# Optimization experiments

Hardware: AMD Instinct MI355X
Metric: run time of the kernel (lower is better)

Reference implementation:

```python
import jax, jax.numpy as jnp
import numpy as np


def setup_inputs() -> dict:
    key = jax.random.key(0)
    ks = jax.random.split(key, 8)
    B, C, H, W = 4, 256, 64, 64
    QP = 32  # query_planes = inplanes // 8
    x = jax.random.normal(ks[0], (B, C, H, W), dtype=jnp.float32)
    Wq = jax.random.normal(ks[1], (QP, C), dtype=jnp.float32) * (1.0 / np.sqrt(C))
    bq = jax.random.normal(ks[2], (QP,), dtype=jnp.float32) * 0.01
    Wk = jax.random.normal(ks[3], (QP, C), dtype=jnp.float32) * (1.0 / np.sqrt(C))
    bk = jax.random.normal(ks[4], (QP,), dtype=jnp.float32) * 0.01
    Wv = jax.random.normal(ks[5], (C, C), dtype=jnp.float32) * (1.0 / np.sqrt(C))
    bv = jax.random.normal(ks[6], (C,), dtype=jnp.float32) * 0.01
    gamma = jax.random.normal(ks[7], (), dtype=jnp.float32)
    return {"x": x, "Wq": Wq, "bq": bq, "Wk": Wk, "bk": bk,
            "Wv": Wv, "bv": bv, "gamma": gamma}


def reference(x, Wq, bq, Wk, bk, Wv, bv, gamma):
    B, C, H, W = x.shape
    N = H * W
    flat = x.reshape(B, C, N)                              # [B, C, N]
    # 1x1 Conv1d == pointwise linear over channel dim
    q = jnp.einsum('qc,bcn->bnq', Wq, flat) + bq[None, None, :]   # [B, N, QP] (already permuted)
    k = jnp.einsum('qc,bcn->bqn', Wk, flat) + bk[None, :, None]   # [B, QP, N]
    v = jnp.einsum('oc,bcn->bon', Wv, flat) + bv[None, :, None]   # [B, C, N]
    # scores[b, i, j] = <q_i, k_j>, NO 1/sqrt(d) scaling (as in source)
    scores = jnp.einsum('biq,bqj->bij', q, k)              # [B, N, N]
    # unusual softmax axis: dim=1 == over query positions i, per column j
    attn = jax.nn.softmax(scores, axis=1)                  # [B, N, N]
    out_attn = jnp.einsum('bcn,bnj->bcj', v, attn)         # [B, C, N]
    out_attn = out_attn.reshape(B, C, H, W)
    return gamma * out_attn + x
```

## Files before the change

### kernel.cpp

```cpp
#include <hip/hip_runtime.h>
#include <hip/hip_bf16.h>
#include <math.h>


#define NBATCH 4
#define CDIM   256
#define NSEQ   4096
#define QPDIM  32
#define LOG2E  1.44269504088896340736f

typedef _Float16 half8_t  __attribute__((ext_vector_type(8)));
typedef _Float16 half2_t  __attribute__((ext_vector_type(2)));
typedef float    floatx4  __attribute__((ext_vector_type(4)));
typedef float    floatx16 __attribute__((ext_vector_type(16)));

union H8 { half8_t h8; half2_t h2[4]; int i32[4]; };

__device__ inline half2_t pack_f16(float a, float b) {
    return __builtin_bit_cast(half2_t, __builtin_amdgcn_cvt_pkrtz(a, b));
}

__global__ __launch_bounds__(256) void wprep_kernel(
    const float* __restrict__ Wv, const float* __restrict__ Wq,
    const float* __restrict__ Wk, _Float16* __restrict__ wH)
{
    const int idx = blockIdx.x * 256 + threadIdx.x;
    const int e = idx * 8;
    const int r = e >> 8, c = e & 255;
    const float* src;
    float scale = 1.0f;
    if (r < 256)      src = Wv + (size_t)r * 256 + c;
    else if (r < 288) { src = Wq + (size_t)(r - 256) * 256 + c; scale = LOG2E; }
    else              src = Wk + (size_t)(r - 288) * 256 + c;
    float4 f0 = ((const float4*)src)[0];
    float4 f1 = ((const float4*)src)[1];
    half8_t h;
    h[0] = (_Float16)(f0.x * scale); h[1] = (_Float16)(f0.y * scale);
    h[2] = (_Float16)(f0.z * scale); h[3] = (_Float16)(f0.w * scale);
    h[4] = (_Float16)(f1.x * scale); h[5] = (_Float16)(f1.y * scale);
    h[6] = (_Float16)(f1.z * scale); h[7] = (_Float16)(f1.w * scale);
    *(half8_t*)(wH + (size_t)r * 256 + c) = h;
}

__global__ __launch_bounds__(256, 2) void qkv_kernel(
    const float* __restrict__ x, const _Float16* __restrict__ wH,
    const float* __restrict__ bq, const float* __restrict__ bk,
    const float* __restrict__ bv,
    _Float16* __restrict__ qH, _Float16* __restrict__ kH,
    _Float16* __restrict__ vHT)
{
    __shared__ _Float16 xT[32][264];

    const int blk  = blockIdx.x;
    const int slot = blk & 7;
    const int b    = slot >> 1;
    const int n0   = (((blk >> 3) << 1) | (slot & 1)) << 5;
    const int t    = threadIdx.x;
    const int w    = t >> 6;
    const int lane = t & 63;
    const int quad = lane >> 4;
    const int col  = lane & 15;

    {
        const int crow0 = t >> 3;
        const int npart = t & 7;
        #pragma unroll
        for (int pass = 0; pass < 8; ++pass) {
            const int c = pass * 32 + crow0;
            float4 f = *(const float4*)(
                x + ((size_t)(b * CDIM + c)) * NSEQ + n0 + npart * 4);
            xT[npart * 4 + 0][c] = (_Float16)f.x;
            xT[npart * 4 + 1][c] = (_Float16)f.y;
            xT[npart * 4 + 2][c] = (_Float16)f.z;
            xT[npart * 4 + 3][c] = (_Float16)f.w;
        }
    }
    __syncthreads();

    const int r0 = w * 80;
    floatx4 acc[5][2];
    #pragma unroll
    for (int mt = 0; mt < 5; ++mt)
        #pragma unroll
        for (int nt = 0; nt < 2; ++nt)
            acc[mt][nt] = (floatx4){0.f, 0.f, 0.f, 0.f};

    #pragma unroll
    for (int ks = 0; ks < 8; ++ks) {
        half8_t bf[2];
        #pragma unroll
        for (int nt = 0; nt < 2; ++nt)
            bf[nt] = *(const half8_t*)&xT[nt * 16 + col][ks * 32 + quad * 8];
        #pragma unroll
        for (int mt = 0; mt < 5; ++mt) {
            half8_t a = *(const half8_t*)(
                wH + (size_t)(r0 + mt * 16 + col) * 256 + ks * 32 + quad * 8);
            #pragma unroll
            for (int nt = 0; nt < 2; ++nt)
                acc[mt][nt] = __builtin_amdgcn_mfma_f32_16x16x32_f16(
                    a, bf[nt], acc[mt][nt], 0, 0, 0);
        }
    }

    #pragma unroll
    for (int mt = 0; mt < 5; ++mt) {
        const int gbase = r0 + mt * 16;
        const float* bp; int rl; float bscale = 1.0f;
        if (gbase < 256)      { bp = bv; rl = gbase; }
        else if (gbase < 288) { bp = bq; rl = gbase - 256; bscale = LOG2E; }
        else                  { bp = bk; rl = gbase - 288; }
        #pragma unroll
        for (int reg = 0; reg < 4; ++reg) {
            const int rr = rl + quad * 4 + reg;
            const float bias = bp[rr] * bscale;
            #pragma unroll
            for (int nt = 0; nt < 2; ++nt) {
                const int n = n0 + nt * 16 + col;
                const float val = acc[mt][nt][reg] + bias;
                if (gbase < 256)
                    vHT[((size_t)(b * CDIM + rr)) * NSEQ + n] = (_Float16)val;
                else if (gbase < 288)
                    qH[((size_t)(b * NSEQ + n)) * QPDIM + rr] = (_Float16)val;
                else
                    kH[((size_t)(b * NSEQ + n)) * QPDIM + rr] = (_Float16)val;
            }
        }
    }
}

__global__ __launch_bounds__(256, 4) void mpass_kernel(
    const _Float16* __restrict__ qH, const _Float16* __restrict__ kH,
    float* __restrict__ ms4)
{
    __shared__ float wmax[4][32];

    const int blk  = blockIdx.x;
    const int slot = blk & 7;
    const int b    = slot >> 1;
    const int idx  = ((blk >> 3) << 1) | (slot & 1);
    const int jblk = idx & 63;
    const int iq   = idx >> 6;
    const int t    = threadIdx.x;
    const int w    = t >> 6;
    const int lane = t & 63;
    const int l5   = lane >> 5;
    const int lj   = lane & 31;
    const int jt   = w & 1, ih = w >> 1;

    const _Float16* qg = qH + (size_t)b * NSEQ * QPDIM;
    const int j = jblk * 64 + jt * 32 + lj;
    const half8_t kb0 = *(const half8_t*)(
        kH + ((size_t)(b * NSEQ + j)) * QPDIM + l5 * 8);
    const half8_t kb1 = *(const half8_t*)(
        kH + ((size_t)(b * NSEQ + j)) * QPDIM + 16 + l5 * 8);

    float mx = -1e30f;
    const int ibase = iq * 1024 + ih * 512;
    for (int cc = 0; cc < 16; ++cc) {
        const _Float16* qp = qg + (size_t)(ibase + cc * 32 + lj) * QPDIM + l5 * 8;
        half8_t qa0 = *(const half8_t*)qp;
        half8_t qa1 = *(const half8_t*)(qp + 16);
        floatx16 S = __builtin_amdgcn_mfma_f32_32x32x16_f16(
            qa0, kb0, (floatx16){0.f}, 0, 0, 0);
        S = __builtin_amdgcn_mfma_f32_32x32x16_f16(qa1, kb1, S, 0, 0, 0);
        #pragma unroll
        for (int r = 0; r < 16; ++r) mx = fmaxf(mx, S[r]);
    }
    mx = fmaxf(mx, __shfl_xor(mx, 32));
    if (lane < 32) wmax[w][lane] = mx;
    __syncthreads();
    if (t < 64) {
        const int jt3 = t >> 5, c = t & 31;
        ms4[(size_t)iq * (NBATCH * NSEQ) + (size_t)b * NSEQ
            + jblk * 64 + jt3 * 32 + c] = fmaxf(wmax[jt3][c], wmax[jt3 + 2][c]);
    }
}

__global__ __launch_bounds__(512, 1) void attn_kernel(
    const _Float16* __restrict__ qH, const _Float16* __restrict__ kH,
    const _Float16* __restrict__ vHT, const float* __restrict__ ms4,
    const float* __restrict__ x, const float* __restrict__ gamma,
    float* __restrict__ out)
{
    __shared__ _Float16 vbuf[2][32768];
    __shared__ float lred[2][4][32];

    const int blk  = blockIdx.x;
    const int slot = blk & 7;
    const int b    = slot >> 1;
    const int jblk = ((blk >> 3) << 1) | (slot & 1);
    const int j0   = jblk << 6;
    const int t    = threadIdx.x;
    const int w    = t >> 6;
    const int lane = t & 63;
    const int l5   = lane >> 5;
    const int lj   = lane & 31;
    const int jh   = w & 1;
    const int ih   = w >> 1;

    const _Float16* qg = qH + (size_t)b * NSEQ * QPDIM;
    const _Float16* vg = vHT + (size_t)b * CDIM * NSEQ;

    const int jme = j0 + jh * 32 + lj;
    const half8_t kb0 = *(const half8_t*)(
        kH + ((size_t)(b * NSEQ + jme)) * QPDIM + l5 * 8);
    const half8_t kb1 = *(const half8_t*)(
        kH + ((size_t)(b * NSEQ + jme)) * QPDIM + 16 + l5 * 8);
    const float* msb = ms4 + (size_t)b * NSEQ + jme;
    const float mfix = fmaxf(
        fmaxf(msb[0], msb[NBATCH * NSEQ]),
        fmaxf(msb[2 * NBATCH * NSEQ], msb[3 * NBATCH * NSEQ]));
    floatx16 Sinit;
    #pragma unroll
    for (int r = 0; r < 16; ++r) Sinit[r] = -mfix;

    floatx16 acc[8];
    #pragma unroll
    for (int ct = 0; ct < 8; ++ct) acc[ct] = (floatx16){0.f};
    float lp = 0.0f;

    #define DMA_V(i0_, buf_)                                                   \
        {                                                                      \
            _Pragma("unroll")                                                  \
            for (int g = 0; g < 8; ++g) {                                      \
                const int uu = w * 512 + g * 64 + lane;                        \
                const int cl = uu >> 4;                                        \
                const int ck = (uu & 15) ^ (cl & 7);                           \
                const _Float16* src =                                          \
                    vg + (size_t)cl * NSEQ + (i0_) + ck * 8;                   \
                __builtin_amdgcn_global_load_lds(                              \
                    (const __attribute__((address_space(1))) void*)src,        \
                    (__attribute__((address_space(3))) void*)                  \
                        (&vbuf[buf_][(w * 512 + g * 64) * 8]),                 \
                    16, 0, 0);                                                 \
            }                                                                  \
        }

    DMA_V(0, 0);
    const _Float16* qb = qg + (size_t)(ih * 32 + lj) * QPDIM + l5 * 8;
    half8_t qa0 = *(const half8_t*)(qb);
    half8_t qa1 = *(const half8_t*)(qb + 16);

    int cur = 0;
    for (int i0 = 0; i0 < NSEQ; i0 += 128) {
        __syncthreads();
        if (i0 + 128 < NSEQ) DMA_V(i0 + 128, cur ^ 1);

        floatx16 S = __builtin_amdgcn_mfma_f32_32x32x16_f16(
            qa0, kb0, Sinit, 0, 0, 0);
        S = __builtin_amdgcn_mfma_f32_32x32x16_f16(qa1, kb1, S, 0, 0, 0);

        H8 lo, hi;
        float ls = 0.0f;
        #pragma unroll
        for (int p = 0; p < 4; ++p) {
            float pa = __builtin_amdgcn_exp2f(S[2 * p]);
            float pb = __builtin_amdgcn_exp2f(S[2 * p + 1]);
            ls += pa + pb;
            lo.h2[p] = pack_f16(pa, pb);
        }
        #pragma unroll
        for (int p = 0; p < 4; ++p) {
            float pa = __builtin_amdgcn_exp2f(S[8 + 2 * p]);
            float pb = __builtin_amdgcn_exp2f(S[8 + 2 * p + 1]);
            ls += pa + pb;
            hi.h2[p] = pack_f16(pa, pb);
        }
        lp += ls;

        H8 P0, P1;
#if __has_builtin(__builtin_amdgcn_permlane32_swap)
        {
            auto r0p = __builtin_amdgcn_permlane32_swap(
                (unsigned)lo.i32[0], (unsigned)lo.i32[2], false, false);
            P0.i32[0] = (int)r0p[0]; P0.i32[2] = (int)r0p[1];
            auto r1p = __builtin_amdgcn_permlane32_swap(
                (unsigned)lo.i32[1], (unsigned)lo.i32[3], false, false);
            P0.i32[1] = (int)r1p[0]; P0.i32[3] = (int)r1p[1];
            auto r2p = __builtin_amdgcn_permlane32_swap(
                (unsigned)hi.i32[0], (unsigned)hi.i32[2], false, false);
            P1.i32[0] = (int)r2p[0]; P1.i32[2] = (int)r2p[1];
            auto r3p = __builtin_amdgcn_permlane32_swap(
                (unsigned)hi.i32[1], (unsigned)hi.i32[3], false, false);
            P1.i32[1] = (int)r3p[0]; P1.i32[3] = (int)r3p[1];
        }
#else
        {
            H8 shl, shh;
            #pragma unroll
            for (int r = 0; r < 4; ++r) {
                shl.i32[r] = __shfl_xor(lo.i32[r], 32);
                shh.i32[r] = __shfl_xor(hi.i32[r], 32);
            }
            const bool high = (l5 != 0);
            P0.i32[0] = high ? shl.i32[2] : lo.i32[0];
            P0.i32[1] = high ? shl.i32[3] : lo.i32[1];
            P0.i32[2] = high ? lo.i32[2]  : shl.i32[0];
            P0.i32[3] = high ? lo.i32[3]  : shl.i32[1];
            P1.i32[0] = high ? shh.i32[2] : hi.i32[0];
            P1.i32[1] = high ? shh.i32[3] : hi.i32[1];
            P1.i32[2] = high ? hi.i32[2]  : shh.i32[0];
            P1.i32[3] = high ? hi.i32[3]  : shh.i32[1];
        }
#endif

        __builtin_amdgcn_s_setprio(1);
        #pragma unroll
        for (int ct = 0; ct < 8; ++ct) {
            const int cl = ct * 32 + lj;
            const int ic0 = (ih * 4 + 0 + l5) ^ (cl & 7);
            const int ic1 = (ih * 4 + 2 + l5) ^ (cl & 7);
            half8_t va0 = *(const half8_t*)&vbuf[cur][(cl * 16 + ic0) * 8];
            half8_t va1 = *(const half8_t*)&vbuf[cur][(cl * 16 + ic1) * 8];
            acc[ct] = __builtin_amdgcn_mfma_f32_32x32x16_f16(
                va0, P0.h8, acc[ct], 0, 0, 0);
            acc[ct] = __builtin_amdgcn_mfma_f32_32x32x16_f16(
                va1, P1.h8, acc[ct], 0, 0, 0);
        }
        __builtin_amdgcn_s_setprio(0);

        if (i0 + 128 < NSEQ) {
            qa0 = *(const half8_t*)(qb + (size_t)(i0 + 128) * QPDIM);
            qa1 = *(const half8_t*)(qb + (size_t)(i0 + 128) * QPDIM + 16);
        }
        cur ^= 1;
    }

    lp += __shfl_xor(lp, 32);
    if (lane < 32) lred[jh][ih][lane] = lp;
    __syncthreads();

    float* fred = (float*)vbuf;
    const int rA = jh * 2 + (ih >> 1);
    if (ih & 1) {
        float* rg = fred + rA * 8192;
        #pragma unroll
        for (int ct = 0; ct < 8; ++ct)
            #pragma unroll
            for (int reg = 0; reg < 16; ++reg) {
                const int crow = (reg & 3) + 8 * (reg >> 2) + 4 * l5;
                rg[(ct * 32 + crow) * 32 + lj] = acc[ct][reg];
            }
    }
    __syncthreads();
    if (!(ih & 1)) {
        float* rg = fred + rA * 8192;
        #pragma unroll
        for (int ct = 0; ct < 8; ++ct)
            #pragma unroll
            for (int reg = 0; reg < 16; ++reg) {
                const int crow = (reg & 3) + 8 * (reg >> 2) + 4 * l5;
                acc[ct][reg] += rg[(ct * 32 + crow) * 32 + lj];
            }
    }
    __syncthreads();
    if (ih == 0) {
        float* rg = fred + (jh * 2 + 0) * 8192;
        #pragma unroll
        for (int ct = 4; ct < 8; ++ct)
            #pragma unroll
            for (int reg = 0; reg < 16; ++reg) {
                const int crow = (reg & 3) + 8 * (reg >> 2) + 4 * l5;
                rg[(ct * 32 + crow) * 32 + lj] = acc[ct][reg];
            }
    } else if (ih == 2) {
        float* rg = fred + (jh * 2 + 1) * 8192;
        #pragma unroll
        for (int ct = 0; ct < 4; ++ct)
            #pragma unroll
            for (int reg = 0; reg < 16; ++reg) {
                const int crow = (reg & 3) + 8 * (reg >> 2) + 4 * l5;
                rg[(ct * 32 + crow) * 32 + lj] = acc[ct][reg];
            }
    }
    __syncthreads();
    if (ih == 0) {
        const float lsum = lred[jh][0][lj] + lred[jh][1][lj]
                         + lred[jh][2][lj] + lred[jh][3][lj];
        const float rv = gamma[0] / lsum;
        float* rg = fred + (jh * 2 + 1) * 8192;
        #pragma unroll
        for (int ct = 0; ct < 4; ++ct) {
            #pragma unroll
            for (int reg = 0; reg < 16; ++reg) {
                const int crow = (reg & 3) + 8 * (reg >> 2) + 4 * l5;
                const int c_ = ct * 32 + crow;
                const size_t off = ((size_t)(b * CDIM + c_)) * NSEQ + jme;
                const float sum =
                    acc[ct][reg] + rg[(ct * 32 + crow) * 32 + lj];
                out[off] = sum * rv + x[off];
            }
        }
    } else if (ih == 2) {
        const float lsum = lred[jh][0][lj] + lred[jh][1][lj]
                         + lred[jh][2][lj] + lred[jh][3][lj];
        const float rv = gamma[0] / lsum;
        float* rg = fred + (jh * 2 + 0) * 8192;
        #pragma unroll
        for (int ct = 4; ct < 8; ++ct) {
            #pragma unroll
            for (int reg = 0; reg < 16; ++reg) {
                const int crow = (reg & 3) + 8 * (reg >> 2) + 4 * l5;
                const int c_ = ct * 32 + crow;
                const size_t off = ((size_t)(b * CDIM + c_)) * NSEQ + jme;
                const float sum =
                    acc[ct][reg] + rg[(ct * 32 + crow) * 32 + lj];
                out[off] = sum * rv + x[off];
            }
        }
    }
}

extern "C" void kernel_launch(void* const* d_in, const int* in_sizes, int n_in,
                              void* d_out, int out_size, void* d_ws, size_t ws_size,
                              hipStream_t stream) {
    const float* x     = (const float*)d_in[0];
    const float* Wq    = (const float*)d_in[1];
    const float* bq    = (const float*)d_in[2];
    const float* Wk    = (const float*)d_in[3];
    const float* bk    = (const float*)d_in[4];
    const float* Wv    = (const float*)d_in[5];
    const float* bv    = (const float*)d_in[6];
    const float* gamma = (const float*)d_in[7];
    float* out = (float*)d_out;

    _Float16* w16 = (_Float16*)d_ws;
    _Float16* qH  = w16;
    _Float16* kH  = qH + (size_t)NBATCH * NSEQ * QPDIM;
    _Float16* vHT = kH + (size_t)NBATCH * NSEQ * QPDIM;
    _Float16* wH  = vHT + (size_t)NBATCH * CDIM * NSEQ;
    float*    ms4 = (float*)(wH + (size_t)320 * 256);

    wprep_kernel<<<40, 256, 0, stream>>>(Wv, Wq, Wk, wH);
    qkv_kernel<<<512, 256, 0, stream>>>(x, wH, bq, bk, bv, qH, kH, vHT);
    mpass_kernel<<<1024, 256, 0, stream>>>(qH, kH, ms4);
    attn_kernel<<<256, 512, 0, stream>>>(qH, kH, vHT, ms4, x, gamma, out);
}
```

Before: 163.7 us.

## Give each warp a private V slice and drop block barriers in attention loop

```diff
diff --git a/kernel.cpp b/kernel.cpp
--- a/kernel.cpp
+++ b/kernel.cpp
@@ -18,6 +18,44 @@
 
 __device__ inline half2_t pack_f16(float a, float b) {
     return __builtin_bit_cast(half2_t, __builtin_amdgcn_cvt_pkrtz(a, b));
+}
+
+__device__ inline void transformP(const H8& lo, const H8& hi,
+                                  H8& P0, H8& P1, const int l5) {
+#if __has_builtin(__builtin_amdgcn_permlane32_swap)
+    {
+        auto r0p = __builtin_amdgcn_permlane32_swap(
+            (unsigned)lo.i32[0], (unsigned)lo.i32[2], false, false);
+        P0.i32[0] = (int)r0p[0]; P0.i32[2] = (int)r0p[1];
+        auto r1p = __builtin_amdgcn_permlane32_swap(
+            (unsigned)lo.i32[1], (unsigned)lo.i32[3], false, false);
+        P0.i32[1] = (int)r1p[0]; P0.i32[3] = (int)r1p[1];
+        auto r2p = __builtin_amdgcn_permlane32_swap(
+            (unsigned)hi.i32[0], (unsigned)hi.i32[2], false, false);
+        P1.i32[0] = (int)r2p[0]; P1.i32[2] = (int)r2p[1];
+        auto r3p = __builtin_amdgcn_permlane32_swap(
+            (unsigned)hi.i32[1], (unsigned)hi.i32[3], false, false);
+        P1.i32[1] = (int)r3p[0]; P1.i32[3] = (int)r3p[1];
+    }
+#else
+    {
+        H8 shl, shh;
+        #pragma unroll
+        for (int r = 0; r < 4; ++r) {
+            shl.i32[r] = __shfl_xor(lo.i32[r], 32);
+            shh.i32[r] = __shfl_xor(hi.i32[r], 32);
+        }
+        const bool high = (l5 != 0);
+        P0.i32[0] = high ? shl.i32[2] : lo.i32[0];
+        P0.i32[1] = high ? shl.i32[3] : lo.i32[1];
+        P0.i32[2] = high ? lo.i32[2]  : shl.i32[0];
+        P0.i32[3] = high ? lo.i32[3]  : shl.i32[1];
+        P1.i32[0] = high ? shh.i32[2] : hi.i32[0];
+        P1.i32[1] = high ? shh.i32[3] : hi.i32[1];
+        P1.i32[2] = high ? hi.i32[2]  : shh.i32[0];
+        P1.i32[3] = high ? hi.i32[3]  : shh.i32[1];
+    }
+#endif
 }
 
 __global__ __launch_bounds__(256) void wprep_kernel(
@@ -183,7 +221,7 @@
     float* __restrict__ out)
 {
     __shared__ _Float16 vbuf[2][32768];
-    __shared__ float lred[2][4][32];
+    __shared__ float lred[4][64];
 
     const int blk  = blockIdx.x;
     const int slot = blk & 7;
@@ -195,39 +233,49 @@
     const int lane = t & 63;
     const int l5   = lane >> 5;
     const int lj   = lane & 31;
-    const int jh   = w & 1;
+    const int ch   = w & 1;
     const int ih   = w >> 1;
 
     const _Float16* qg = qH + (size_t)b * NSEQ * QPDIM;
     const _Float16* vg = vHT + (size_t)b * CDIM * NSEQ;
 
-    const int jme = j0 + jh * 32 + lj;
-    const half8_t kb0 = *(const half8_t*)(
-        kH + ((size_t)(b * NSEQ + jme)) * QPDIM + l5 * 8);
-    const half8_t kb1 = *(const half8_t*)(
-        kH + ((size_t)(b * NSEQ + jme)) * QPDIM + 16 + l5 * 8);
-    const float* msb = ms4 + (size_t)b * NSEQ + jme;
-    const float mfix = fmaxf(
-        fmaxf(msb[0], msb[NBATCH * NSEQ]),
-        fmaxf(msb[2 * NBATCH * NSEQ], msb[3 * NBATCH * NSEQ]));
-    floatx16 Sinit;
+    const int jme0 = j0 + lj;
+    const int jme1 = j0 + 32 + lj;
+    const half8_t kbA0 = *(const half8_t*)(
+        kH + ((size_t)(b * NSEQ + jme0)) * QPDIM + l5 * 8);
+    const half8_t kbB0 = *(const half8_t*)(
+        kH + ((size_t)(b * NSEQ + jme0)) * QPDIM + 16 + l5 * 8);
+    const half8_t kbA1 = *(const half8_t*)(
+        kH + ((size_t)(b * NSEQ + jme1)) * QPDIM + l5 * 8);
+    const half8_t kbB1 = *(const half8_t*)(
+        kH + ((size_t)(b * NSEQ + jme1)) * QPDIM + 16 + l5 * 8);
+
+    const float* msb0 = ms4 + (size_t)b * NSEQ + jme0;
+    const float mf0 = fmaxf(
+        fmaxf(msb0[0], msb0[NBATCH * NSEQ]),
+        fmaxf(msb0[2 * NBATCH * NSEQ], msb0[3 * NBATCH * NSEQ]));
+    const float* msb1 = ms4 + (size_t)b * NSEQ + jme1;
+    const float mf1 = fmaxf(
+        fmaxf(msb1[0], msb1[NBATCH * NSEQ]),
+        fmaxf(msb1[2 * NBATCH * NSEQ], msb1[3 * NBATCH * NSEQ]));
+
+    floatx16 acc[4][2];
     #pragma unroll
-    for (int r = 0; r < 16; ++r) Sinit[r] = -mfix;
-
-    floatx16 acc[8];
-    #pragma unroll
-    for (int ct = 0; ct < 8; ++ct) acc[ct] = (floatx16){0.f};
-    float lp = 0.0f;
+    for (int ct = 0; ct < 4; ++ct)
+        #pragma unroll
+        for (int jt = 0; jt < 2; ++jt) acc[ct][jt] = (floatx16){0.f};
+    float lp0 = 0.0f, lp1 = 0.0f;
 
     #define DMA_V(i0_, buf_)                                                   \
         {                                                                      \
             _Pragma("unroll")                                                  \
             for (int g = 0; g < 8; ++g) {                                      \
-                const int uu = w * 512 + g * 64 + lane;                        \
-                const int cl = uu >> 4;                                        \
-                const int ck = (uu & 15) ^ (cl & 7);                           \
+                const int uu = g * 64 + lane;                                  \
+                const int cl = uu >> 2;                                        \
+                const int ck = (uu & 3) ^ ((cl >> 1) & 3);                     \
                 const _Float16* src =                                          \
-                    vg + (size_t)cl * NSEQ + (i0_) + ck * 8;                   \
+                    vg + (size_t)(ch * 128 + cl) * NSEQ + (i0_) + ih * 32      \
+                       + ck * 8;                                               \
                 __builtin_amdgcn_global_load_lds(                              \
                     (const __attribute__((address_space(1))) void*)src,        \
                     (__attribute__((address_space(3))) void*)                  \
@@ -243,81 +291,93 @@
 
     int cur = 0;
     for (int i0 = 0; i0 < NSEQ; i0 += 128) {
-        __syncthreads();
-        if (i0 + 128 < NSEQ) DMA_V(i0 + 128, cur ^ 1);
-
-        floatx16 S = __builtin_amdgcn_mfma_f32_32x32x16_f16(
-            qa0, kb0, Sinit, 0, 0, 0);
-        S = __builtin_amdgcn_mfma_f32_32x32x16_f16(qa1, kb1, S, 0, 0, 0);
-
-        H8 lo, hi;
-        float ls = 0.0f;
-        #pragma unroll
-        for (int p = 0; p < 4; ++p) {
-            float pa = __builtin_amdgcn_exp2f(S[2 * p]);
-            float pb = __builtin_amdgcn_exp2f(S[2 * p + 1]);
-            ls += pa + pb;
-            lo.h2[p] = pack_f16(pa, pb);
-        }
-        #pragma unroll
-        for (int p = 0; p < 4; ++p) {
-            float pa = __builtin_amdgcn_exp2f(S[8 + 2 * p]);
-            float pb = __builtin_amdgcn_exp2f(S[8 + 2 * p + 1]);
-            ls += pa + pb;
-            hi.h2[p] = pack_f16(pa, pb);
-        }
-        lp += ls;
-
-        H8 P0, P1;
-#if __has_builtin(__builtin_amdgcn_permlane32_swap)
+        if (i0 + 128 < NSEQ) {
+            DMA_V(i0 + 128, cur ^ 1);
+            asm volatile("s_waitcnt vmcnt(8)" ::: "memory");
+        } else {
+            asm volatile("s_waitcnt vmcnt(0)" ::: "memory");
+        }
+        __builtin_amdgcn_sched_barrier(0);
+
+        half8_t va[4][2];
+        #pragma unroll
+        for (int ct = 0; ct < 4; ++ct) {
+            const int clr = ct * 32 + lj;
+            const int sw  = (clr >> 1) & 3;
+            va[ct][0] = *(const half8_t*)
+                &vbuf[cur][(w * 512 + clr * 4 + ((0 + l5) ^ sw)) * 8];
+            va[ct][1] = *(const half8_t*)
+                &vbuf[cur][(w * 512 + clr * 4 + ((2 + l5) ^ sw)) * 8];
+        }
+
+        floatx16 S0 = __builtin_amdgcn_mfma_f32_32x32x16_f16(
+            qa0, kbA0, (floatx16){0.f}, 0, 0, 0);
+        S0 = __builtin_amdgcn_mfma_f32_32x32x16_f16(qa1, kbB0, S0, 0, 0, 0);
+        floatx16 S1 = __builtin_amdgcn_mfma_f32_32x32x16_f16(
+            qa0, kbA1, (floatx16){0.f}, 0, 0, 0);
+        S1 = __builtin_amdgcn_mfma_f32_32x32x16_f16(qa1, kbB1, S1, 0, 0, 0);
+
         {
-            auto r0p = __builtin_amdgcn_permlane32_swap(
-                (unsigned)lo.i32[0], (unsigned)lo.i32[2], false, false);
-            P0.i32[0] = (int)r0p[0]; P0.i32[2] = (int)r0p[1];
-            auto r1p = __builtin_amdgcn_permlane32_swap(
-                (unsigned)lo.i32[1], (unsigned)lo.i32[3], false, false);
-            P0.i32[1] = (int)r1p[0]; P0.i32[3] = (int)r1p[1];
-            auto r2p = __builtin_amdgcn_permlane32_swap(
-                (unsigned)hi.i32[0], (unsigned)hi.i32[2], false, false);
-            P1.i32[0] = (int)r2p[0]; P1.i32[2] = (int)r2p[1];
-            auto r3p = __builtin_amdgcn_permlane32_swap(
-                (unsigned)hi.i32[1], (unsigned)hi.i32[3], false, false);
-            P1.i32[1] = (int)r3p[0]; P1.i32[3] = (int)r3p[1];
-        }
-#else
+            H8 lo, hi;
+            float ls = 0.0f;
+            #pragma unroll
+            for (int p = 0; p < 4; ++p) {
+                float pa = __builtin_amdgcn_exp2f(S0[2 * p]     - mf0);
+                float pb = __builtin_amdgcn_exp2f(S0[2 * p + 1] - mf0);
+                ls += pa + pb;
+                lo.h2[p] = pack_f16(pa, pb);
+            }
+            #pragma unroll
+            for (int p = 0; p < 4; ++p) {
+                float pa = __builtin_amdgcn_exp2f(S0[8 + 2 * p]     - mf0);
+                float pb = __builtin_amdgcn_exp2f(S0[8 + 2 * p + 1] - mf0);
+                ls += pa + pb;
+                hi.h2[p] = pack_f16(pa, pb);
+            }
+            lp0 += ls;
+            H8 Pa, Pb;
+            transformP(lo, hi, Pa, Pb, l5);
+            __builtin_amdgcn_s_setprio(1);
+            #pragma unroll
+            for (int ct = 0; ct < 4; ++ct) {
+                acc[ct][0] = __builtin_amdgcn_mfma_f32_32x32x16_f16(
+                    va[ct][0], Pa.h8, acc[ct][0], 0, 0, 0);
+                acc[ct][0] = __builtin_amdgcn_mfma_f32_32x32x16_f16(
+                    va[ct][1], Pb.h8, acc[ct][0], 0, 0, 0);
+            }
+            __builtin_amdgcn_s_setprio(0);
+        }
+
         {
-            H8 shl, shh;
-            #pragma unroll
-            for (int r = 0; r < 4; ++r) {
-                shl.i32[r] = __shfl_xor(lo.i32[r], 32);
-                shh.i32[r] = __shfl_xor(hi.i32[r], 32);
-            }
-            const bool high = (l5 != 0);
-            P0.i32[0] = high ? shl.i32[2] : lo.i32[0];
-            P0.i32[1] = high ? shl.i32[3] : lo.i32[1];
-            P0.i32[2] = high ? lo.i32[2]  : shl.i32[0];
-            P0.i32[3] = high ? lo.i32[3]  : shl.i32[1];
-            P1.i32[0] = high ? shh.i32[2] : hi.i32[0];
-            P1.i32[1] = high ? shh.i32[3] : hi.i32[1];
-            P1.i32[2] = high ? hi.i32[2]  : shh.i32[0];
-            P1.i32[3] = high ? hi.i32[3]  : shh.i32[1];
-        }
-#endif
-
-        __builtin_amdgcn_s_setprio(1);
-        #pragma unroll
-        for (int ct = 0; ct < 8; ++ct) {
-            const int cl = ct * 32 + lj;
-            const int ic0 = (ih * 4 + 0 + l5) ^ (cl & 7);
-            const int ic1 = (ih * 4 + 2 + l5) ^ (cl & 7);
-            half8_t va0 = *(const half8_t*)&vbuf[cur][(cl * 16 + ic0) * 8];
-            half8_t va1 = *(const half8_t*)&vbuf[cur][(cl * 16 + ic1) * 8];
-            acc[ct] = __builtin_amdgcn_mfma_f32_32x32x16_f16(
-                va0, P0.h8, acc[ct], 0, 0, 0);
-            acc[ct] = __builtin_amdgcn_mfma_f32_32x32x16_f16(
-                va1, P1.h8, acc[ct], 0, 0, 0);
-        }
-        __builtin_amdgcn_s_setprio(0);
+            H8 lo, hi;
+            float ls = 0.0f;
+            #pragma unroll
+            for (int p = 0; p < 4; ++p) {
+                float pa = __builtin_amdgcn_exp2f(S1[2 * p]     - mf1);
+                float pb = __builtin_amdgcn_exp2f(S1[2 * p + 1] - mf1);
+                ls += pa + pb;
+                lo.h2[p] = pack_f16(pa, pb);
+            }
+            #pragma unroll
+            for (int p = 0; p < 4; ++p) {
+                float pa = __builtin_amdgcn_exp2f(S1[8 + 2 * p]     - mf1);
+                float pb = __builtin_amdgcn_exp2f(S1[8 + 2 * p + 1] - mf1);
+                ls += pa + pb;
+                hi.h2[p] = pack_f16(pa, pb);
+            }
+            lp1 += ls;
+            H8 Pa, Pb;
+            transformP(lo, hi, Pa, Pb, l5);
+            __builtin_amdgcn_s_setprio(1);
+            #pragma unroll
+            for (int ct = 0; ct < 4; ++ct) {
+                acc[ct][1] = __builtin_amdgcn_mfma_f32_32x32x16_f16(
+                    va[ct][0], Pa.h8, acc[ct][1], 0, 0, 0);
+                acc[ct][1] = __builtin_amdgcn_mfma_f32_32x32x16_f16(
+                    va[ct][1], Pb.h8, acc[ct][1], 0, 0, 0);
+            }
+            __builtin_amdgcn_s_setprio(0);
+        }
 
         if (i0 + 128 < NSEQ) {
             qa0 = *(const half8_t*)(qb + (size_t)(i0 + 128) * QPDIM);
@@ -326,88 +386,108 @@
         cur ^= 1;
     }
 
-    lp += __shfl_xor(lp, 32);
-    if (lane < 32) lred[jh][ih][lane] = lp;
+    lp0 += __shfl_xor(lp0, 32);
+    lp1 += __shfl_xor(lp1, 32);
+    if (ch == 0 && lane < 32) {
+        lred[ih][lane]      = lp0;
+        lred[ih][32 + lane] = lp1;
+    }
     __syncthreads();
 
     float* fred = (float*)vbuf;
-    const int rA = jh * 2 + (ih >> 1);
     if (ih & 1) {
-        float* rg = fred + rA * 8192;
-        #pragma unroll
-        for (int ct = 0; ct < 8; ++ct)
-            #pragma unroll
-            for (int reg = 0; reg < 16; ++reg) {
-                const int crow = (reg & 3) + 8 * (reg >> 2) + 4 * l5;
-                rg[(ct * 32 + crow) * 32 + lj] = acc[ct][reg];
-            }
+        float* rg = fred + (ch * 2 + (ih >> 1)) * 8192;
+        #pragma unroll
+        for (int ct = 0; ct < 4; ++ct)
+            #pragma unroll
+            for (int jt = 0; jt < 2; ++jt)
+                #pragma unroll
+                for (int reg = 0; reg < 16; ++reg) {
+                    const int crow = (reg & 3) + 8 * (reg >> 2) + 4 * l5;
+                    rg[((ct * 2 + jt) * 32 + crow) * 32 + lj] = acc[ct][jt][reg];
+                }
     }
     __syncthreads();
     if (!(ih & 1)) {
-        float* rg = fred + rA * 8192;
-        #pragma unroll
-        for (int ct = 0; ct < 8; ++ct)
-            #pragma unroll
-            for (int reg = 0; reg < 16; ++reg) {
-                const int crow = (reg & 3) + 8 * (reg >> 2) + 4 * l5;
-                acc[ct][reg] += rg[(ct * 32 + crow) * 32 + lj];
-            }
+        float* rg = fred + (ch * 2 + (ih >> 1)) * 8192;
+        #pragma unroll
+        for (int ct = 0; ct < 4; ++ct)
+            #pragma unroll
+            for (int jt = 0; jt < 2; ++jt)
+                #pragma unroll
+                for (int reg = 0; reg < 16; ++reg) {
+                    const int crow = (reg & 3) + 8 * (reg >> 2) + 4 * l5;
+                    acc[ct][jt][reg] += rg[((ct * 2 + jt) * 32 + crow) * 32 + lj];
+                }
     }
     __syncthreads();
     if (ih == 0) {
-        float* rg = fred + (jh * 2 + 0) * 8192;
-        #pragma unroll
-        for (int ct = 4; ct < 8; ++ct)
-            #pragma unroll
-            for (int reg = 0; reg < 16; ++reg) {
-                const int crow = (reg & 3) + 8 * (reg >> 2) + 4 * l5;
-                rg[(ct * 32 + crow) * 32 + lj] = acc[ct][reg];
-            }
+        float* rg = fred + (ch * 2 + 0) * 8192;
+        #pragma unroll
+        for (int ct = 2; ct < 4; ++ct)
+            #pragma unroll
+            for (int jt = 0; jt < 2; ++jt)
+                #pragma unroll
+                for (int reg = 0; reg < 16; ++reg) {
+                    const int crow = (reg & 3) + 8 * (reg >> 2) + 4 * l5;
+                    rg[(((ct - 2) * 2 + jt) * 32 + crow) * 32 + lj] =
+                        acc[ct][jt][reg];
+                }
     } else if (ih == 2) {
-        float* rg = fred + (jh * 2 + 1) * 8192;
-        #pragma unroll
-        for (int ct = 0; ct < 4; ++ct)
-            #pragma unroll
-            for (int reg = 0; reg < 16; ++reg) {
-                const int crow = (reg & 3) + 8 * (reg >> 2) + 4 * l5;
-                rg[(ct * 32 + crow) * 32 + lj] = acc[ct][reg];
-            }
+        float* rg = fred + (ch * 2 + 1) * 8192;
+        #pragma unroll
+        for (int ct = 0; ct < 2; ++ct)
+            #pragma unroll
+            for (int jt = 0; jt < 2; ++jt)
+                #pragma unroll
+                for (int reg = 0; reg < 16; ++reg) {
+                    const int crow = (reg & 3) + 8 * (reg >> 2) + 4 * l5;
+                    rg[((ct * 2 + jt) * 32 + crow) * 32 + lj] = acc[ct][jt][reg];
+                }
     }
     __syncthreads();
     if (ih == 0) {
-        const float lsum = lred[jh][0][lj] + lred[jh][1][lj]
-                         + lred[jh][2][lj] + lred[jh][3][lj];
-        const float rv = gamma[0] / lsum;
-        float* rg = fred + (jh * 2 + 1) * 8192;
-        #pragma unroll
-        for (int ct = 0; ct < 4; ++ct) {
-            #pragma unroll
-            for (int reg = 0; reg < 16; ++reg) {
-                const int crow = (reg & 3) + 8 * (reg >> 2) + 4 * l5;
-                const int c_ = ct * 32 + crow;
-                const size_t off = ((size_t)(b * CDIM + c_)) * NSEQ + jme;
-                const float sum =
-                    acc[ct][reg] + rg[(ct * 32 + crow) * 32 + lj];
-                out[off] = sum * rv + x[off];
-            }
-        }
+        const float l0 = lred[0][lj] + lred[1][lj] + lred[2][lj] + lred[3][lj];
+        const float l1 = lred[0][32 + lj] + lred[1][32 + lj]
+                       + lred[2][32 + lj] + lred[3][32 + lj];
+        const float rv0 = gamma[0] / l0;
+        const float rv1 = gamma[0] / l1;
+        float* rg = fred + (ch * 2 + 1) * 8192;
+        #pragma unroll
+        for (int ct = 0; ct < 2; ++ct)
+            #pragma unroll
+            for (int jt = 0; jt < 2; ++jt)
+                #pragma unroll
+                for (int reg = 0; reg < 16; ++reg) {
+                    const int crow = (reg & 3) + 8 * (reg >> 2) + 4 * l5;
+                    const int c_ = ch * 128 + ct * 32 + crow;
+                    const int j_ = jt ? jme1 : jme0;
+                    const size_t off = ((size_t)(b * CDIM + c_)) * NSEQ + j_;
+                    const float sum = acc[ct][jt][reg]
+                        + rg[((ct * 2 + jt) * 32 + crow) * 32 + lj];
+                    out[off] = sum * (jt ? rv1 : rv0) + x[off];
+                }
     } else if (ih == 2) {
-        const float lsum = lred[jh][0][lj] + lred[jh][1][lj]
-                         + lred[jh][2][lj] + lred[jh][3][lj];
-        const float rv = gamma[0] / lsum;
-        float* rg = fred + (jh * 2 + 0) * 8192;
-        #pragma unroll
-        for (int ct = 4; ct < 8; ++ct) {
-            #pragma unroll
-            for (int reg = 0; reg < 16; ++reg) {
-                const int crow = (reg & 3) + 8 * (reg >> 2) + 4 * l5;
-                const int c_ = ct * 32 + crow;
-                const size_t off = ((size_t)(b * CDIM + c_)) * NSEQ + jme;
-                const float sum =
-                    acc[ct][reg] + rg[(ct * 32 + crow) * 32 + lj];
-                out[off] = sum * rv + x[off];
-            }
-        }
+        const float l0 = lred[0][lj] + lred[1][lj] + lred[2][lj] + lred[3][lj];
+        const float l1 = lred[0][32 + lj] + lred[1][32 + lj]
+                       + lred[2][32 + lj] + lred[3][32 + lj];
+        const float rv0 = gamma[0] / l0;
+        const float rv1 = gamma[0] / l1;
+        float* rg = fred + (ch * 2 + 0) * 8192;
+        #pragma unroll
+        for (int ct = 2; ct < 4; ++ct)
+            #pragma unroll
+            for (int jt = 0; jt < 2; ++jt)
+                #pragma unroll
+                for (int reg = 0; reg < 16; ++reg) {
+                    const int crow = (reg & 3) + 8 * (reg >> 2) + 4 * l5;
+                    const int c_ = ch * 128 + ct * 32 + crow;
+                    const int j_ = jt ? jme1 : jme0;
+                    const size_t off = ((size_t)(b * CDIM + c_)) * NSEQ + j_;
+                    const float sum = acc[ct][jt][reg]
+                        + rg[(((ct - 2) * 2 + jt) * 32 + crow) * 32 + lj];
+                    out[off] = sum * (jt ? rv1 : rv0) + x[off];
+                }
     }
 }
 
```

Result: slower. 218.6 us (+33.6%).

## Load V directly from global into registers and split attention blocks per column half

Applied to the files above, without the earlier changes.

```diff
diff --git a/kernel.cpp b/kernel.cpp
--- a/kernel.cpp
+++ b/kernel.cpp
@@ -18,6 +18,44 @@
 
 __device__ inline half2_t pack_f16(float a, float b) {
     return __builtin_bit_cast(half2_t, __builtin_amdgcn_cvt_pkrtz(a, b));
+}
+
+__device__ inline void transformP(const H8& lo, const H8& hi,
+                                  H8& P0, H8& P1, const int l5) {
+#if __has_builtin(__builtin_amdgcn_permlane32_swap)
+    {
+        auto r0p = __builtin_amdgcn_permlane32_swap(
+            (unsigned)lo.i32[0], (unsigned)lo.i32[2], false, false);
+        P0.i32[0] = (int)r0p[0]; P0.i32[2] = (int)r0p[1];
+        auto r1p = __builtin_amdgcn_permlane32_swap(
+            (unsigned)lo.i32[1], (unsigned)lo.i32[3], false, false);
+        P0.i32[1] = (int)r1p[0]; P0.i32[3] = (int)r1p[1];
+        auto r2p = __builtin_amdgcn_permlane32_swap(
+            (unsigned)hi.i32[0], (unsigned)hi.i32[2], false, false);
+        P1.i32[0] = (int)r2p[0]; P1.i32[2] = (int)r2p[1];
+        auto r3p = __builtin_amdgcn_permlane32_swap(
+            (unsigned)hi.i32[1], (unsigned)hi.i32[3], false, false);
+        P1.i32[1] = (int)r3p[0]; P1.i32[3] = (int)r3p[1];
+    }
+#else
+    {
+        H8 shl, shh;
+        #pragma unroll
+        for (int r = 0; r < 4; ++r) {
+            shl.i32[r] = __shfl_xor(lo.i32[r], 32);
+            shh.i32[r] = __shfl_xor(hi.i32[r], 32);
+        }
+        const bool high = (l5 != 0);
+        P0.i32[0] = high ? shl.i32[2] : lo.i32[0];
+        P0.i32[1] = high ? shl.i32[3] : lo.i32[1];
+        P0.i32[2] = high ? lo.i32[2]  : shl.i32[0];
+        P0.i32[3] = high ? lo.i32[3]  : shl.i32[1];
+        P1.i32[0] = high ? shh.i32[2] : hi.i32[0];
+        P1.i32[1] = high ? shh.i32[3] : hi.i32[1];
+        P1.i32[2] = high ? hi.i32[2]  : shh.i32[0];
+        P1.i32[3] = high ? hi.i32[3]  : shh.i32[1];
+    }
+#endif
 }
 
 __global__ __launch_bounds__(256) void wprep_kernel(
@@ -176,32 +214,31 @@
     }
 }
 
-__global__ __launch_bounds__(512, 1) void attn_kernel(
+__global__ __launch_bounds__(256, 2) void attn_kernel(
     const _Float16* __restrict__ qH, const _Float16* __restrict__ kH,
     const _Float16* __restrict__ vHT, const float* __restrict__ ms4,
     const float* __restrict__ x, const float* __restrict__ gamma,
     float* __restrict__ out)
 {
-    __shared__ _Float16 vbuf[2][32768];
-    __shared__ float lred[2][4][32];
+    __shared__ float fred[2][8192];
+    __shared__ float lred[4][32];
 
     const int blk  = blockIdx.x;
     const int slot = blk & 7;
     const int b    = slot >> 1;
-    const int jblk = ((blk >> 3) << 1) | (slot & 1);
-    const int j0   = jblk << 6;
+    const int jh   = slot & 1;
+    const int jblk = blk >> 3;
+    const int j0   = jblk * 64 + jh * 32;
     const int t    = threadIdx.x;
-    const int w    = t >> 6;
     const int lane = t & 63;
     const int l5   = lane >> 5;
     const int lj   = lane & 31;
-    const int jh   = w & 1;
-    const int ih   = w >> 1;
+    const int ih   = t >> 6;
 
     const _Float16* qg = qH + (size_t)b * NSEQ * QPDIM;
     const _Float16* vg = vHT + (size_t)b * CDIM * NSEQ;
 
-    const int jme = j0 + jh * 32 + lj;
+    const int jme = j0 + lj;
     const half8_t kb0 = *(const half8_t*)(
         kH + ((size_t)(b * NSEQ + jme)) * QPDIM + l5 * 8);
     const half8_t kb1 = *(const half8_t*)(
@@ -219,32 +256,21 @@
     for (int ct = 0; ct < 8; ++ct) acc[ct] = (floatx16){0.f};
     float lp = 0.0f;
 
-    #define DMA_V(i0_, buf_)                                                   \
-        {                                                                      \
-            _Pragma("unroll")                                                  \
-            for (int g = 0; g < 8; ++g) {                                      \
-                const int uu = w * 512 + g * 64 + lane;                        \
-                const int cl = uu >> 4;                                        \
-                const int ck = (uu & 15) ^ (cl & 7);                           \
-                const _Float16* src =                                          \
-                    vg + (size_t)cl * NSEQ + (i0_) + ck * 8;                   \
-                __builtin_amdgcn_global_load_lds(                              \
-                    (const __attribute__((address_space(1))) void*)src,        \
-                    (__attribute__((address_space(3))) void*)                  \
-                        (&vbuf[buf_][(w * 512 + g * 64) * 8]),                 \
-                    16, 0, 0);                                                 \
-            }                                                                  \
-        }
-
-    DMA_V(0, 0);
     const _Float16* qb = qg + (size_t)(ih * 32 + lj) * QPDIM + l5 * 8;
-    half8_t qa0 = *(const half8_t*)(qb);
-    half8_t qa1 = *(const half8_t*)(qb + 16);
-
-    int cur = 0;
+
     for (int i0 = 0; i0 < NSEQ; i0 += 128) {
-        __syncthreads();
-        if (i0 + 128 < NSEQ) DMA_V(i0 + 128, cur ^ 1);
+        const int ib = i0 + ih * 32;
+
+        half8_t qa0 = *(const half8_t*)(qb + (size_t)i0 * QPDIM);
+        half8_t qa1 = *(const half8_t*)(qb + (size_t)i0 * QPDIM + 16);
+
+        half8_t vaA[4][2];
+        #pragma unroll
+        for (int ct = 0; ct < 4; ++ct) {
+            const _Float16* vp = vg + (size_t)(ct * 32 + lj) * NSEQ + ib + l5 * 8;
+            vaA[ct][0] = *(const half8_t*)(vp);
+            vaA[ct][1] = *(const half8_t*)(vp + 16);
+        }
 
         floatx16 S = __builtin_amdgcn_mfma_f32_32x32x16_f16(
             qa0, kb0, Sinit, 0, 0, 0);
@@ -268,72 +294,42 @@
         }
         lp += ls;
 
-        H8 P0, P1;
-#if __has_builtin(__builtin_amdgcn_permlane32_swap)
-        {
-            auto r0p = __builtin_amdgcn_permlane32_swap(
-                (unsigned)lo.i32[0], (unsigned)lo.i32[2], false, false);
-            P0.i32[0] = (int)r0p[0]; P0.i32[2] = (int)r0p[1];
-            auto r1p = __builtin_amdgcn_permlane32_swap(
-                (unsigned)lo.i32[1], (unsigned)lo.i32[3], false, false);
-            P0.i32[1] = (int)r1p[0]; P0.i32[3] = (int)r1p[1];
-            auto r2p = __builtin_amdgcn_permlane32_swap(
-                (unsigned)hi.i32[0], (unsigned)hi.i32[2], false, false);
-            P1.i32[0] = (int)r2p[0]; P1.i32[2] = (int)r2p[1];
-            auto r3p = __builtin_amdgcn_permlane32_swap(
-                (unsigned)hi.i32[1], (unsigned)hi.i32[3], false, false);
-            P1.i32[1] = (int)r3p[0]; P1.i32[3] = (int)r3p[1];
-        }
-#else
-        {
-            H8 shl, shh;
-            #pragma unroll
-            for (int r = 0; r < 4; ++r) {
-                shl.i32[r] = __shfl_xor(lo.i32[r], 32);
-                shh.i32[r] = __shfl_xor(hi.i32[r], 32);
-            }
-            const bool high = (l5 != 0);
-            P0.i32[0] = high ? shl.i32[2] : lo.i32[0];
-            P0.i32[1] = high ? shl.i32[3] : lo.i32[1];
-            P0.i32[2] = high ? lo.i32[2]  : shl.i32[0];
-            P0.i32[3] = high ? lo.i32[3]  : shl.i32[1];
-            P1.i32[0] = high ? shh.i32[2] : hi.i32[0];
-            P1.i32[1] = high ? shh.i32[3] : hi.i32[1];
-            P1.i32[2] = high ? hi.i32[2]  : shh.i32[0];
-            P1.i32[3] = high ? hi.i32[3]  : shh.i32[1];
-        }
-#endif
+        H8 Pa, Pb;
+        transformP(lo, hi, Pa, Pb, l5);
+
+        half8_t vaB[4][2];
+        #pragma unroll
+        for (int ct = 0; ct < 4; ++ct) {
+            const _Float16* vp =
+                vg + (size_t)((ct + 4) * 32 + lj) * NSEQ + ib + l5 * 8;
+            vaB[ct][0] = *(const half8_t*)(vp);
+            vaB[ct][1] = *(const half8_t*)(vp + 16);
+        }
 
         __builtin_amdgcn_s_setprio(1);
         #pragma unroll
-        for (int ct = 0; ct < 8; ++ct) {
-            const int cl = ct * 32 + lj;
-            const int ic0 = (ih * 4 + 0 + l5) ^ (cl & 7);
-            const int ic1 = (ih * 4 + 2 + l5) ^ (cl & 7);
-            half8_t va0 = *(const half8_t*)&vbuf[cur][(cl * 16 + ic0) * 8];
-            half8_t va1 = *(const half8_t*)&vbuf[cur][(cl * 16 + ic1) * 8];
+        for (int ct = 0; ct < 4; ++ct) {
             acc[ct] = __builtin_amdgcn_mfma_f32_32x32x16_f16(
-                va0, P0.h8, acc[ct], 0, 0, 0);
+                vaA[ct][0], Pa.h8, acc[ct], 0, 0, 0);
             acc[ct] = __builtin_amdgcn_mfma_f32_32x32x16_f16(
-                va1, P1.h8, acc[ct], 0, 0, 0);
+                vaA[ct][1], Pb.h8, acc[ct], 0, 0, 0);
+        }
+        #pragma unroll
+        for (int ct = 0; ct < 4; ++ct) {
+            acc[ct + 4] = __builtin_amdgcn_mfma_f32_32x32x16_f16(
+                vaB[ct][0], Pa.h8, acc[ct + 4], 0, 0, 0);
+            acc[ct + 4] = __builtin_amdgcn_mfma_f32_32x32x16_f16(
+                vaB[ct][1], Pb.h8, acc[ct + 4], 0, 0, 0);
         }
         __builtin_amdgcn_s_setprio(0);
-
-        if (i0 + 128 < NSEQ) {
-            qa0 = *(const half8_t*)(qb + (size_t)(i0 + 128) * QPDIM);
-            qa1 = *(const half8_t*)(qb + (size_t)(i0 + 128) * QPDIM + 16);
-        }
-        cur ^= 1;
     }
 
     lp += __shfl_xor(lp, 32);
-    if (lane < 32) lred[jh][ih][lane] = lp;
-    __syncthreads();
-
-    float* fred = (float*)vbuf;
-    const int rA = jh * 2 + (ih >> 1);
+    if (lane < 32) lred[ih][lane] = lp;
+    __syncthreads();
+
     if (ih & 1) {
-        float* rg = fred + rA * 8192;
+        float* rg = fred[ih >> 1];
         #pragma unroll
         for (int ct = 0; ct < 8; ++ct)
             #pragma unroll
@@ -344,7 +340,7 @@
     }
     __syncthreads();
     if (!(ih & 1)) {
-        float* rg = fred + rA * 8192;
+        float* rg = fred[ih >> 1];
         #pragma unroll
         for (int ct = 0; ct < 8; ++ct)
             #pragma unroll
@@ -355,7 +351,7 @@
     }
     __syncthreads();
     if (ih == 0) {
-        float* rg = fred + (jh * 2 + 0) * 8192;
+        float* rg = fred[0];
         #pragma unroll
         for (int ct = 4; ct < 8; ++ct)
             #pragma unroll
@@ -364,7 +360,7 @@
                 rg[(ct * 32 + crow) * 32 + lj] = acc[ct][reg];
             }
     } else if (ih == 2) {
-        float* rg = fred + (jh * 2 + 1) * 8192;
+        float* rg = fred[1];
         #pragma unroll
         for (int ct = 0; ct < 4; ++ct)
             #pragma unroll
@@ -375,10 +371,9 @@
     }
     __syncthreads();
     if (ih == 0) {
-        const float lsum = lred[jh][0][lj] + lred[jh][1][lj]
-                         + lred[jh][2][lj] + lred[jh][3][lj];
+        const float lsum = lred[0][lj] + lred[1][lj] + lred[2][lj] + lred[3][lj];
         const float rv = gamma[0] / lsum;
-        float* rg = fred + (jh * 2 + 1) * 8192;
+        float* rg = fred[1];
         #pragma unroll
         for (int ct = 0; ct < 4; ++ct) {
             #pragma unroll
@@ -392,10 +387,9 @@
             }
         }
     } else if (ih == 2) {
-        const float lsum = lred[jh][0][lj] + lred[jh][1][lj]
-                         + lred[jh][2][lj] + lred[jh][3][lj];
+        const float lsum = lred[0][lj] + lred[1][lj] + lred[2][lj] + lred[3][lj];
         const float rv = gamma[0] / lsum;
-        float* rg = fred + (jh * 2 + 0) * 8192;
+        float* rg = fred[0];
         #pragma unroll
         for (int ct = 4; ct < 8; ++ct) {
             #pragma unroll
@@ -434,5 +428,5 @@
     wprep_kernel<<<40, 256, 0, stream>>>(Wv, Wq, Wk, wH);
     qkv_kernel<<<512, 256, 0, stream>>>(x, wH, bq, bk, bv, qH, kH, vHT);
     mpass_kernel<<<1024, 256, 0, stream>>>(qH, kH, ms4);
-    attn_kernel<<<256, 512, 0, stream>>>(qH, kH, vHT, ms4, x, gamma, out);
-}
+    attn_kernel<<<512, 256, 0, stream>>>(qH, kH, vHT, ms4, x, gamma, out);
+}
```

New measurement: 234.3 us. 43.2% more time.
